# Optimization experiments

Hardware: AMD Instinct MI355X
Metric: run time of the kernel (lower is better)

Reference implementation:

```python
import jax, jax.numpy as jnp
import numpy as np

NEG_SLOPE = 0.01  # F.leaky_relu default


def setup_inputs() -> dict:
    key = jax.random.key(0)
    k1, k2, k3, k4, k5, k6 = jax.random.split(key, 6)
    N, E, IN, OUT = 100000, 1600000, 128, 64
    return {
        "h": jax.random.normal(k1, (N, IN), dtype=jnp.float32),
        "src": jax.random.randint(k2, (E,), 0, N, dtype=jnp.int32),
        "dst": jax.random.randint(k3, (E,), 0, N, dtype=jnp.int32),
        "W_fc": jax.random.normal(k4, (IN, OUT), dtype=jnp.float32) * (1.0 / np.sqrt(IN)),
        "a_l": jax.random.normal(k5, (OUT,), dtype=jnp.float32) * (1.0 / np.sqrt(2 * OUT)),
        "a_r": jax.random.normal(k6, (OUT,), dtype=jnp.float32) * (1.0 / np.sqrt(2 * OUT)),
    }


def reference(h, src, dst, W_fc, a_l, a_r):
    N = h.shape[0]
    # z = fc(h)  (no bias)
    z = h @ W_fc                                  # [N, D]
    # attn_fc(cat(z_src, z_dst)) == z_src @ a_l + z_dst @ a_r
    s = z @ a_l                                   # [N]
    t = z @ a_r                                   # [N]
    e = jax.nn.leaky_relu(s[src] + t[dst], NEG_SLOPE)  # [E]
    # segment (per-destination-node) softmax over incoming edges
    m = jax.ops.segment_max(e, dst, num_segments=N)    # [N]
    ex = jnp.exp(e - m[dst])                            # [E]
    denom = jax.ops.segment_sum(ex, dst, num_segments=N)  # [N]
    alpha = ex / denom[dst]                              # [E]
    # weighted scatter-sum of source features
    out = jax.ops.segment_sum(alpha[:, None] * z[src], dst, num_segments=N)  # [N, D]
    return out
```

## Files before the change

kernel.cpp:

```cpp
#include <hip/hip_runtime.h>
#include <math.h>

#define IN_DIM 128
#define OUT_DIM 64
#define NEG_SLOPE 0.01f

__global__ void init_kernel(int* __restrict__ count, int N) {
  int i = blockIdx.x * blockDim.x + threadIdx.x;
  if (i < N) count[i] = 0;
}

__global__ __launch_bounds__(256) void fc_kernel(
    const float* __restrict__ h, const float* __restrict__ W,
    const float* __restrict__ al, const float* __restrict__ ar,
    float* __restrict__ z, float* __restrict__ s, float* __restrict__ t, int N) {
  __shared__ float hlds[64][IN_DIM];
  int tid = threadIdx.x;
  int nb = blockIdx.x * 64;

  for (int it = tid; it < 64 * (IN_DIM / 4); it += 256) {
    int r = it >> 5;
    int kq = it & 31;
    int row = nb + r;
    float4 v = make_float4(0.f, 0.f, 0.f, 0.f);
    if (row < N) v = *(const float4*)&h[(size_t)row * IN_DIM + kq * 4];
    *(float4*)&hlds[r][kq * 4] = v;
  }
  __syncthreads();

  int lane = tid & 63, wid = tid >> 6;
  int n0 = wid * 16;
  float acc[16];
#pragma unroll
  for (int i = 0; i < 16; ++i) acc[i] = 0.f;

  for (int kq = 0; kq < IN_DIM / 4; ++kq) {
    int k = kq * 4;
    float w0 = W[(size_t)(k + 0) * OUT_DIM + lane];
    float w1 = W[(size_t)(k + 1) * OUT_DIM + lane];
    float w2 = W[(size_t)(k + 2) * OUT_DIM + lane];
    float w3 = W[(size_t)(k + 3) * OUT_DIM + lane];
#pragma unroll
    for (int nn = 0; nn < 16; ++nn) {
      float4 hv = *(const float4*)&hlds[n0 + nn][k];
      float a = acc[nn];
      a = fmaf(hv.x, w0, a);
      a = fmaf(hv.y, w1, a);
      a = fmaf(hv.z, w2, a);
      a = fmaf(hv.w, w3, a);
      acc[nn] = a;
    }
  }

  float alv = al[lane], arv = ar[lane];
#pragma unroll
  for (int nn = 0; nn < 16; ++nn) {
    int row = nb + n0 + nn;
    float p = acc[nn] * alv;
    float q = acc[nn] * arv;
#pragma unroll
    for (int off = 32; off; off >>= 1) {
      p += __shfl_down(p, off);
      q += __shfl_down(q, off);
    }
    if (row < N) {
      z[(size_t)row * OUT_DIM + lane] = acc[nn];
      if (lane == 0) { s[row] = p; t[row] = q; }
    }
  }
}

__global__ void edge_pass1(const int* __restrict__ dst, int* __restrict__ count,
                           int* __restrict__ rank, int E) {
  int i = blockIdx.x * blockDim.x + threadIdx.x;
  if (i < E) rank[i] = atomicAdd(&count[dst[i]], 1);
}

__global__ __launch_bounds__(256) void scan_block_sums(const int* __restrict__ count, int N,
                                                       int* __restrict__ bsums) {
  int b = blockIdx.x, tid = threadIdx.x;
  int base = b * 2048;
  int sum = 0;
  for (int i = tid; i < 2048; i += 256) {
    int idx = base + i;
    if (idx < N) sum += count[idx];
  }
#pragma unroll
  for (int off = 32; off; off >>= 1) sum += __shfl_down(sum, off);
  __shared__ int ws[4];
  int lane = tid & 63, wid = tid >> 6;
  if (lane == 0) ws[wid] = sum;
  __syncthreads();
  if (tid == 0) bsums[b] = ws[0] + ws[1] + ws[2] + ws[3];
}

__global__ void scan_bsums(const int* __restrict__ bsums, int nb, int* __restrict__ bofs,
                           int* __restrict__ offs, int N, int E) {
  if (blockIdx.x == 0 && threadIdx.x == 0) {
    int run = 0;
    for (int i = 0; i < nb; ++i) { bofs[i] = run; run += bsums[i]; }
    offs[N] = E;
  }
}

__global__ __launch_bounds__(256) void scan_write(const int* __restrict__ count, int N,
                                                  const int* __restrict__ bofs,
                                                  int* __restrict__ offs) {
  int b = blockIdx.x, tid = threadIdx.x;
  int base = b * 2048 + tid * 8;
  int v[8];
  int tot = 0;
#pragma unroll
  for (int i = 0; i < 8; ++i) {
    int idx = base + i;
    int c = (idx < N) ? count[idx] : 0;
    v[i] = c;
    tot += c;
  }
  int lane = tid & 63, wid = tid >> 6;
  int x = tot;
#pragma unroll
  for (int off = 1; off < 64; off <<= 1) {
    int y = __shfl_up(x, off);
    if (lane >= off) x += y;
  }
  __shared__ int wtot[4];
  if (lane == 63) wtot[wid] = x;
  __syncthreads();
  int wbase = 0;
  for (int w2 = 0; w2 < wid; ++w2) wbase += wtot[w2];
  int run = bofs[b] + wbase + (x - tot);
#pragma unroll
  for (int i = 0; i < 8; ++i) {
    int idx = base + i;
    if (idx < N) offs[idx] = run;
    run += v[i];
  }
}

__global__ void edge_pass2(const int* __restrict__ src, const int* __restrict__ dst,
                           const int* __restrict__ rank, const int* __restrict__ offs,
                           int* __restrict__ csr_src, int E) {
  int i = blockIdx.x * blockDim.x + threadIdx.x;
  if (i >= E) return;
  int d = dst[i];
  csr_src[offs[d] + rank[i]] = src[i];
}

__global__ __launch_bounds__(256) void aggregate_kernel(
    const int* __restrict__ offs, const int* __restrict__ csr_src,
    const float* __restrict__ s, const float* __restrict__ t,
    const float* __restrict__ z, float* __restrict__ out, int N) {
  int wid = threadIdx.x >> 6, lane = threadIdx.x & 63;
  int n = blockIdx.x * 4 + wid;
  if (n >= N) return;
  int beg = offs[n], end = offs[n + 1];
  int deg = end - beg;
  float acc = 0.f;

  if (deg > 0 && deg <= 64) {
    float tn = t[n];
    float e_l = -INFINITY;
    int sn_l = 0;
    if (lane < deg) {
      sn_l = csr_src[beg + lane];
      float e = s[sn_l] + tn;
      e_l = e > 0.f ? e : NEG_SLOPE * e;
    }
    float mn = e_l;
#pragma unroll
    for (int off = 32; off; off >>= 1) mn = fmaxf(mn, __shfl_xor(mn, off));
    float w_l = (lane < deg) ? __expf(e_l - mn) : 0.f;
    float wsum = w_l;
#pragma unroll
    for (int off = 32; off; off >>= 1) wsum += __shfl_xor(wsum, off);
    int k = 0;
    for (; k + 4 <= deg; k += 4) {
      int s0 = __shfl(sn_l, k + 0), s1 = __shfl(sn_l, k + 1);
      int s2 = __shfl(sn_l, k + 2), s3 = __shfl(sn_l, k + 3);
      float w0 = __shfl(w_l, k + 0), w1 = __shfl(w_l, k + 1);
      float w2 = __shfl(w_l, k + 2), w3 = __shfl(w_l, k + 3);
      float z0 = z[(size_t)s0 * OUT_DIM + lane];
      float z1 = z[(size_t)s1 * OUT_DIM + lane];
      float z2 = z[(size_t)s2 * OUT_DIM + lane];
      float z3 = z[(size_t)s3 * OUT_DIM + lane];
      acc = fmaf(w0, z0, acc);
      acc = fmaf(w1, z1, acc);
      acc = fmaf(w2, z2, acc);
      acc = fmaf(w3, z3, acc);
    }
    for (; k < deg; ++k) {
      int s0 = __shfl(sn_l, k);
      float w0 = __shfl(w_l, k);
      acc = fmaf(w0, z[(size_t)s0 * OUT_DIM + lane], acc);
    }
    acc /= wsum;
  } else if (deg > 64) {
    float tn = t[n];
    float mn = -INFINITY;
    for (int p = beg + lane; p < end; p += 64) {
      float e = s[csr_src[p]] + tn;
      e = e > 0.f ? e : NEG_SLOPE * e;
      mn = fmaxf(mn, e);
    }
#pragma unroll
    for (int off = 32; off; off >>= 1) mn = fmaxf(mn, __shfl_xor(mn, off));
    float wsum = 0.f;
    for (int p = beg; p < end; ++p) {
      int sn = csr_src[p];
      float e = s[sn] + tn;
      e = e > 0.f ? e : NEG_SLOPE * e;
      float w = __expf(e - mn);
      wsum += w;
      acc = fmaf(w, z[(size_t)sn * OUT_DIM + lane], acc);
    }
    acc /= wsum;
  }
  out[(size_t)n * OUT_DIM + lane] = acc;
}

extern "C" void kernel_launch(void* const* d_in, const int* in_sizes, int n_in,
                              void* d_out, int out_size, void* d_ws, size_t ws_size,
                              hipStream_t stream) {
  const float* h = (const float*)d_in[0];
  const int* src = (const int*)d_in[1];
  const int* dst = (const int*)d_in[2];
  const float* W = (const float*)d_in[3];
  const float* al = (const float*)d_in[4];
  const float* ar = (const float*)d_in[5];
  float* out = (float*)d_out;
  int N = in_sizes[0] / IN_DIM;
  int E = in_sizes[1];

  float* z = (float*)d_ws;
  float* s = z + (size_t)N * OUT_DIM;
  float* t = s + N;
  int* count = (int*)(t + N);
  int* offs = count + N;
  int* rank = offs + N + 1;
  int* csr_src = rank + E;
  int* bsums = csr_src + E;
  int* bofs = bsums + 256;

  const int NB = (N + 2047) / 2048;

  hipLaunchKernelGGL(init_kernel, dim3((N + 255) / 256), dim3(256), 0, stream, count, N);
  hipLaunchKernelGGL(fc_kernel, dim3((N + 63) / 64), dim3(256), 0, stream, h, W, al, ar, z, s, t, N);
  hipLaunchKernelGGL(edge_pass1, dim3((E + 255) / 256), dim3(256), 0, stream, dst, count, rank, E);
  hipLaunchKernelGGL(scan_block_sums, dim3(NB), dim3(256), 0, stream, count, N, bsums);
  hipLaunchKernelGGL(scan_bsums, dim3(1), dim3(64), 0, stream, bsums, NB, bofs, offs, N, E);
  hipLaunchKernelGGL(scan_write, dim3(NB), dim3(256), 0, stream, count, N, bofs, offs);
  hipLaunchKernelGGL(edge_pass2, dim3((E + 255) / 256), dim3(256), 0, stream, src, dst, rank, offs, csr_src, E);
  hipLaunchKernelGGL(aggregate_kernel, dim3((N + 3) / 4), dim3(256), 0, stream, offs, csr_src, s, t, z, out, N);
}
```

Baseline: 330.2 us.

## Fuse GEMM with edge counting, merge scan stages, vectorize aggregation gather

Merges the fc GEMM and the edge-counting atomic pass into one launch with interleaved block roles, so the atomic-bound pass overlaps the compute-bound GEMM. It replaces the init kernel with a memset and folds the single-thread block-sum scan into scan_write, where every block redundantly scans the block sums in LDS. The aggregation for low-degree nodes now gathers float4 rows with four edge groups per wavefront and reduces them with shuffles, giving wider loads and fewer load instructions. Costs are extra shuffle reductions, padded edge iterations, and interleaved block scheduling that could unbalance work.

```diff
diff --git a/kernel.cpp b/kernel.cpp
--- a/kernel.cpp
+++ b/kernel.cpp
@@ -5,18 +5,27 @@
 #define OUT_DIM 64
 #define NEG_SLOPE 0.01f
 
-__global__ void init_kernel(int* __restrict__ count, int N) {
-  int i = blockIdx.x * blockDim.x + threadIdx.x;
-  if (i < N) count[i] = 0;
-}
-
-__global__ __launch_bounds__(256) void fc_kernel(
+__global__ __launch_bounds__(256) void fc_edge_kernel(
     const float* __restrict__ h, const float* __restrict__ W,
     const float* __restrict__ al, const float* __restrict__ ar,
-    float* __restrict__ z, float* __restrict__ s, float* __restrict__ t, int N) {
+    const int* __restrict__ dst,
+    float* __restrict__ z, float* __restrict__ s, float* __restrict__ t,
+    int* __restrict__ count, int* __restrict__ rank,
+    int N, int E, int nGemm, int nEdge) {
   __shared__ float hlds[64][IN_DIM];
+  int b = blockIdx.x;
   int tid = threadIdx.x;
-  int nb = blockIdx.x * 64;
+  bool isGemm = ((b & 3) == 0) && ((b >> 2) < nGemm);
+
+  if (!isGemm) {
+    int eb = b - min((b + 3) >> 2, nGemm);
+    int stride = nEdge * 256;
+    for (int i = eb * 256 + tid; i < E; i += stride)
+      rank[i] = atomicAdd(&count[dst[i]], 1);
+    return;
+  }
+
+  int nb = (b >> 2) * 64;
 
   for (int it = tid; it < 64 * (IN_DIM / 4); it += 256) {
     int r = it >> 5;
@@ -70,12 +79,6 @@
   }
 }
 
-__global__ void edge_pass1(const int* __restrict__ dst, int* __restrict__ count,
-                           int* __restrict__ rank, int E) {
-  int i = blockIdx.x * blockDim.x + threadIdx.x;
-  if (i < E) rank[i] = atomicAdd(&count[dst[i]], 1);
-}
-
 __global__ __launch_bounds__(256) void scan_block_sums(const int* __restrict__ count, int N,
                                                        int* __restrict__ bsums) {
   int b = blockIdx.x, tid = threadIdx.x;
@@ -94,19 +97,32 @@
   if (tid == 0) bsums[b] = ws[0] + ws[1] + ws[2] + ws[3];
 }
 
-__global__ void scan_bsums(const int* __restrict__ bsums, int nb, int* __restrict__ bofs,
-                           int* __restrict__ offs, int N, int E) {
-  if (blockIdx.x == 0 && threadIdx.x == 0) {
-    int run = 0;
-    for (int i = 0; i < nb; ++i) { bofs[i] = run; run += bsums[i]; }
-    offs[N] = E;
-  }
-}
-
 __global__ __launch_bounds__(256) void scan_write(const int* __restrict__ count, int N,
-                                                  const int* __restrict__ bofs,
-                                                  int* __restrict__ offs) {
-  int b = blockIdx.x, tid = threadIdx.x;
+                                                  const int* __restrict__ bsums, int NB,
+                                                  int* __restrict__ offs, int E) {
+  __shared__ int sb[256];
+  __shared__ int wtot4[4];
+  int tid = threadIdx.x, lane = tid & 63, wid = tid >> 6;
+
+  int v0 = (tid < NB) ? bsums[tid] : 0;
+  int x0 = v0;
+#pragma unroll
+  for (int off = 1; off < 64; off <<= 1) {
+    int y = __shfl_up(x0, off);
+    if (lane >= off) x0 += y;
+  }
+  if (lane == 63) wtot4[wid] = x0;
+  __syncthreads();
+  int wb = 0;
+  for (int w = 0; w < wid; ++w) wb += wtot4[w];
+  sb[tid] = x0 - v0 + wb;
+  __syncthreads();
+
+  int b = blockIdx.x;
+  int bofs = sb[b];
+  if (b == 0 && tid == 0) offs[N] = E;
+  __syncthreads();
+
   int base = b * 2048 + tid * 8;
   int v[8];
   int tot = 0;
@@ -117,7 +133,6 @@
     v[i] = c;
     tot += c;
   }
-  int lane = tid & 63, wid = tid >> 6;
   int x = tot;
 #pragma unroll
   for (int off = 1; off < 64; off <<= 1) {
@@ -129,7 +144,7 @@
   __syncthreads();
   int wbase = 0;
   for (int w2 = 0; w2 < wid; ++w2) wbase += wtot[w2];
-  int run = bofs[b] + wbase + (x - tot);
+  int run = bofs + wbase + (x - tot);
 #pragma unroll
   for (int i = 0; i < 8; ++i) {
     int idx = base + i;
@@ -156,7 +171,6 @@
   if (n >= N) return;
   int beg = offs[n], end = offs[n + 1];
   int deg = end - beg;
-  float acc = 0.f;
 
   if (deg > 0 && deg <= 64) {
     float tn = t[n];
@@ -174,27 +188,33 @@
     float wsum = w_l;
 #pragma unroll
     for (int off = 32; off; off >>= 1) wsum += __shfl_xor(wsum, off);
-    int k = 0;
-    for (; k + 4 <= deg; k += 4) {
-      int s0 = __shfl(sn_l, k + 0), s1 = __shfl(sn_l, k + 1);
-      int s2 = __shfl(sn_l, k + 2), s3 = __shfl(sn_l, k + 3);
-      float w0 = __shfl(w_l, k + 0), w1 = __shfl(w_l, k + 1);
-      float w2 = __shfl(w_l, k + 2), w3 = __shfl(w_l, k + 3);
-      float z0 = z[(size_t)s0 * OUT_DIM + lane];
-      float z1 = z[(size_t)s1 * OUT_DIM + lane];
-      float z2 = z[(size_t)s2 * OUT_DIM + lane];
-      float z3 = z[(size_t)s3 * OUT_DIM + lane];
-      acc = fmaf(w0, z0, acc);
-      acc = fmaf(w1, z1, acc);
-      acc = fmaf(w2, z2, acc);
-      acc = fmaf(w3, z3, acc);
-    }
-    for (; k < deg; ++k) {
-      int s0 = __shfl(sn_l, k);
-      float w0 = __shfl(w_l, k);
-      acc = fmaf(w0, z[(size_t)s0 * OUT_DIM + lane], acc);
-    }
-    acc /= wsum;
+    float inv = 1.0f / wsum;
+
+    int g = lane >> 4, c = lane & 15;
+    float4 a4 = make_float4(0.f, 0.f, 0.f, 0.f);
+    int degR = (deg + 7) & ~7;
+    for (int k = 0; k < degR; k += 8) {
+      int i1 = k + g, i2 = k + 4 + g;
+      int s1 = __shfl(sn_l, i1), s2 = __shfl(sn_l, i2);
+      float w1 = __shfl(w_l, i1), w2 = __shfl(w_l, i2);
+      float4 v1 = *(const float4*)&z[(size_t)s1 * OUT_DIM + c * 4];
+      float4 v2 = *(const float4*)&z[(size_t)s2 * OUT_DIM + c * 4];
+      a4.x = fmaf(w1, v1.x, a4.x); a4.y = fmaf(w1, v1.y, a4.y);
+      a4.z = fmaf(w1, v1.z, a4.z); a4.w = fmaf(w1, v1.w, a4.w);
+      a4.x = fmaf(w2, v2.x, a4.x); a4.y = fmaf(w2, v2.y, a4.y);
+      a4.z = fmaf(w2, v2.z, a4.z); a4.w = fmaf(w2, v2.w, a4.w);
+    }
+#pragma unroll
+    for (int off = 16; off <= 32; off <<= 1) {
+      a4.x += __shfl_xor(a4.x, off);
+      a4.y += __shfl_xor(a4.y, off);
+      a4.z += __shfl_xor(a4.z, off);
+      a4.w += __shfl_xor(a4.w, off);
+    }
+    if (lane < 16) {
+      a4.x *= inv; a4.y *= inv; a4.z *= inv; a4.w *= inv;
+      *(float4*)&out[(size_t)n * OUT_DIM + lane * 4] = a4;
+    }
   } else if (deg > 64) {
     float tn = t[n];
     float mn = -INFINITY;
@@ -206,6 +226,7 @@
 #pragma unroll
     for (int off = 32; off; off >>= 1) mn = fmaxf(mn, __shfl_xor(mn, off));
     float wsum = 0.f;
+    float acc = 0.f;
     for (int p = beg; p < end; ++p) {
       int sn = csr_src[p];
       float e = s[sn] + tn;
@@ -214,9 +235,11 @@
       wsum += w;
       acc = fmaf(w, z[(size_t)sn * OUT_DIM + lane], acc);
     }
-    acc /= wsum;
-  }
-  out[(size_t)n * OUT_DIM + lane] = acc;
+    out[(size_t)n * OUT_DIM + lane] = acc / wsum;
+  } else {
+    if (lane < 16)
+      *(float4*)&out[(size_t)n * OUT_DIM + lane * 4] = make_float4(0.f, 0.f, 0.f, 0.f);
+  }
 }
 
 extern "C" void kernel_launch(void* const* d_in, const int* in_sizes, int n_in,
@@ -240,16 +263,17 @@
   int* rank = offs + N + 1;
   int* csr_src = rank + E;
   int* bsums = csr_src + E;
-  int* bofs = bsums + 256;
 
   const int NB = (N + 2047) / 2048;
-
-  hipLaunchKernelGGL(init_kernel, dim3((N + 255) / 256), dim3(256), 0, stream, count, N);
-  hipLaunchKernelGGL(fc_kernel, dim3((N + 63) / 64), dim3(256), 0, stream, h, W, al, ar, z, s, t, N);
-  hipLaunchKernelGGL(edge_pass1, dim3((E + 255) / 256), dim3(256), 0, stream, dst, count, rank, E);
+  const int nGemm = (N + 63) / 64;
+  const int nEdge = 3 * nGemm;
+  const int nTotal = nGemm + nEdge;
+
+  hipMemsetAsync(count, 0, (size_t)N * sizeof(int), stream);
+  hipLaunchKernelGGL(fc_edge_kernel, dim3(nTotal), dim3(256), 0, stream,
+                     h, W, al, ar, dst, z, s, t, count, rank, N, E, nGemm, nEdge);
   hipLaunchKernelGGL(scan_block_sums, dim3(NB), dim3(256), 0, stream, count, N, bsums);
-  hipLaunchKernelGGL(scan_bsums, dim3(1), dim3(64), 0, stream, bsums, NB, bofs, offs, N, E);
-  hipLaunchKernelGGL(scan_write, dim3(NB), dim3(256), 0, stream, count, N, bofs, offs);
+  hipLaunchKernelGGL(scan_write, dim3(NB), dim3(256), 0, stream, count, N, bsums, NB, offs, E);
   hipLaunchKernelGGL(edge_pass2, dim3((E + 255) / 256), dim3(256), 0, stream, src, dst, rank, offs, csr_src, E);
   hipLaunchKernelGGL(aggregate_kernel, dim3((N + 3) / 4), dim3(256), 0, stream, offs, csr_src, s, t, z, out, N);
 }
```

Measured after the change: 376.3 us. 1.14x slower.
